# Optimization experiments

Hardware: AMD Instinct MI355X
Metric: run time of the kernel (lower is better)

## Reference

```python
import jax, jax.numpy as jnp
import numpy as np

T = 2048        # num tokens
HID = 2048      # hidden_size
HQ = 16         # num_heads
HKV = 8         # num_kv_heads
D = 128         # head_dim
P = 2           # power retention exponent
THETA = 10000.0 # rope base
SCALE = D ** -0.5


def setup_inputs() -> dict:
    key = jax.random.key(0)
    ks = jax.random.split(key, 8)
    s = 0.02
    return {
        "positions": jnp.arange(T, dtype=jnp.int64) if jax.config.jax_enable_x64 else jnp.arange(T, dtype=jnp.int32),
        "hidden_states": jax.random.normal(ks[0], (T, HID), jnp.float32),
        "Wq": jax.random.normal(ks[1], (HID, HQ * D), jnp.float32) * s,
        "bq": jnp.zeros((HQ * D,), jnp.float32),
        "Wk": jax.random.normal(ks[2], (HID, HKV * D), jnp.float32) * s,
        "bk": jnp.zeros((HKV * D,), jnp.float32),
        "Wv": jax.random.normal(ks[3], (HID, HKV * D), jnp.float32) * s,
        "bv": jnp.zeros((HKV * D,), jnp.float32),
        "Wg": jax.random.normal(ks[4], (HID, HKV), jnp.float32) * s,
        "bg": jnp.zeros((HKV,), jnp.float32),
        "Wo": jax.random.normal(ks[5], (HQ * D, HID), jnp.float32) * s,
        "bo": jnp.zeros((HID,), jnp.float32),
    }


def _rope_neox(x, pos):
    # x: [T, H, D], pos: [T]; rotate-half (neox) style, rotary_dim == head_dim
    half = D // 2
    inv_freq = 1.0 / (THETA ** (jnp.arange(0, D, 2, dtype=jnp.float32) / D))  # [D/2]
    freqs = pos.astype(jnp.float32)[:, None] * inv_freq                        # [T, D/2]
    cos = jnp.cos(freqs)[:, None, :]
    sin = jnp.sin(freqs)[:, None, :]
    x1, x2 = x[..., :half], x[..., half:]
    return jnp.concatenate([x1 * cos - x2 * sin, x2 * cos + x1 * sin], axis=-1)


def reference(positions, hidden_states, Wq, bq, Wk, bk, Wv, bv, Wg, bg, Wo, bo):
    # QKVG projections
    q = (hidden_states @ Wq + bq).reshape(T, HQ, D)
    k = (hidden_states @ Wk + bk).reshape(T, HKV, D)
    v = (hidden_states @ Wv + bv).reshape(T, HKV, D)
    g = hidden_states @ Wg + bg            # [T, HKV], one gate scalar per kv head

    # RoPE on q/k, logsigmoid gate in fp32
    q = _rope_neox(q, positions)
    k = _rope_neox(k, positions)
    g = jax.nn.log_sigmoid(g.astype(jnp.float32))   # [T, HKV], <= 0
    G = jnp.cumsum(g, axis=0)                       # [T, HKV] cumulative log-decay

    # GQA: expand kv heads to query heads
    rep = HQ // HKV
    k = jnp.repeat(k, rep, axis=1)   # [T, HQ, D]
    v = jnp.repeat(v, rep, axis=1)
    G = jnp.repeat(G, rep, axis=1)   # [T, HQ]

    # Power retention (quadratic attention form, seq_len <= switch_over_seq_len):
    # W_ij = (scale * q_i . k_j)^p * exp(G_i - G_j), causal j <= i
    S = jnp.einsum('thd,shd->hts', q, k) * SCALE      # [H, T, T]
    S = S ** P
    Gh = G.T                                          # [H, T]
    mask = jnp.tril(jnp.ones((T, T), dtype=bool))
    diff = jnp.where(mask[None], Gh[:, :, None] - Gh[:, None, :], -jnp.inf)
    W = S * jnp.exp(diff)                             # decay<=1 inside mask, 0 outside

    out = jnp.einsum('hts,shd->thd', W, v)            # [T, H, D]
    out = out.reshape(T, HQ * D) @ Wo + bo            # o_proj
    return out
```

## Files before the change

kernel.cpp:

```cpp
#include <hip/hip_runtime.h>
#include <hip/hip_bf16.h>
#include <math.h>

#define T_SEQ 2048
#define HID 2048
#define HQ 16
#define HKV 8
#define D_HEAD 128
#define HALF 64
#define SCALE_F 0.08838834764831845f
#define PROJW 4096

typedef __attribute__((ext_vector_type(8))) short bf16x8;
typedef __attribute__((ext_vector_type(4))) float f32x4;

static __device__ __forceinline__ short f2bf(float x) {
  unsigned u = __builtin_bit_cast(unsigned, x);
  unsigned r = (u + 0x7FFF + ((u >> 16) & 1)) >> 16;
  return (short)r;
}
static __device__ __forceinline__ float bf2f(unsigned short u) {
  unsigned v = ((unsigned)u) << 16;
  return __builtin_bit_cast(float, v);
}

#define GLDS(gsrc, ldst) \
  __builtin_amdgcn_global_load_lds((const __attribute__((address_space(1))) void*)(gsrc), \
                                   (__attribute__((address_space(3))) void*)(ldst), 16, 0, 0)

__global__ __launch_bounds__(256)
void transpose_all(const float* __restrict__ Wq, const float* __restrict__ Wk,
                   const float* __restrict__ Wv, const float* __restrict__ Wo,
                   short* __restrict__ BTall, short* __restrict__ WoT)
{
  const int bx = blockIdx.x;
  const int k0 = blockIdx.y * 32;
  const float* src; short* dst; int Nsrc, n0;
  if (bx < 64)       { src = Wq; Nsrc = 2048; dst = BTall;                       n0 = bx * 32; }
  else if (bx < 96)  { src = Wk; Nsrc = 1024; dst = BTall + (size_t)2048 * 2048; n0 = (bx - 64) * 32; }
  else if (bx < 128) { src = Wv; Nsrc = 1024; dst = BTall + (size_t)3072 * 2048; n0 = (bx - 96) * 32; }
  else               { src = Wo; Nsrc = 2048; dst = WoT;                         n0 = (bx - 128) * 32; }

  __shared__ float tile[32][33];
  const int r = threadIdx.x >> 5, c = threadIdx.x & 31;
  #pragma unroll
  for (int i = 0; i < 4; ++i)
    tile[r + i * 8][c] = src[(size_t)(k0 + r + i * 8) * Nsrc + n0 + c];
  __syncthreads();
  const int n = threadIdx.x >> 3, k4 = (threadIdx.x & 7) * 4;
  short4 o;
  o.x = f2bf(tile[k4 + 0][n]); o.y = f2bf(tile[k4 + 1][n]);
  o.z = f2bf(tile[k4 + 2][n]); o.w = f2bf(tile[k4 + 3][n]);
  *reinterpret_cast<short4*>(&dst[(size_t)(n0 + n) * 2048 + k0 + k4]) = o;
}

__global__ __launch_bounds__(256)
void add_f32(float* __restrict__ out, const float* __restrict__ part, int n4)
{
  int i = blockIdx.x * blockDim.x + threadIdx.x;
  if (i >= n4) return;
  float4 a = reinterpret_cast<float4*>(out)[i];
  const float4 b = reinterpret_cast<const float4*>(part)[i];
  a.x += b.x; a.y += b.y; a.z += b.z; a.w += b.w;
  reinterpret_cast<float4*>(out)[i] = a;
}

template <bool OBF>
__global__ __launch_bounds__(256)
void gemm_bf16(const short* __restrict__ A, const short* __restrict__ BT,
               const float* __restrict__ b0, const float* __restrict__ b1,
               const float* __restrict__ b2, int s1, int s2,
               void* __restrict__ Cout0, void* __restrict__ Cout1,
               int N, int Kst, int klen)
{
  __shared__ short As[2][128 * 32];
  __shared__ short Bs[2][128 * 32];
  const int tid = threadIdx.x;
  const int wave = tid >> 6, lane = tid & 63;
  const int bm0 = blockIdx.y * 128, bn0 = blockIdx.x * 128;
  const int z = blockIdx.z;
  const int koff = z * klen;
  const int wm = (wave >> 1) * 64, wn = (wave & 1) * 64;

  const int srow = wave * 32 + (lane >> 2);
  const int scol = (lane & 3) * 8;
  const short* Abase = A + (size_t)(bm0 + srow) * Kst + koff + scol;
  const short* Bbase = BT + (size_t)(bn0 + srow) * Kst + koff + scol;

  f32x4 acc[4][4] = {};

  const int nk = klen >> 5;
#define STAGE(buf, k0)                                                           \
  do {                                                                           \
    GLDS(Abase + (k0), &As[buf][(wave * 32) * 32]);                              \
    GLDS(Abase + (k0) + (size_t)16 * Kst, &As[buf][(wave * 32 + 16) * 32]);      \
    GLDS(Bbase + (k0), &Bs[buf][(wave * 32) * 32]);                              \
    GLDS(Bbase + (k0) + (size_t)16 * Kst, &Bs[buf][(wave * 32 + 16) * 32]);      \
  } while (0)

  STAGE(0, 0);
  __syncthreads();

  const int kof = (lane >> 4) * 8;
  const int rA = wm + (lane & 15);
  const int rB = wn + (lane & 15);

  for (int t = 0; t < nk; ++t) {
    const int cur = t & 1;
    if (t + 1 < nk) STAGE(cur ^ 1, (t + 1) << 5);
    bf16x8 af[4], bfr[4];
    #pragma unroll
    for (int i = 0; i < 4; ++i) {
      af[i]  = *reinterpret_cast<const bf16x8*>(&As[cur][(rA + i * 16) * 32 + kof]);
      bfr[i] = *reinterpret_cast<const bf16x8*>(&Bs[cur][(rB + i * 16) * 32 + kof]);
    }
    #pragma unroll
    for (int i = 0; i < 4; ++i)
      #pragma unroll
      for (int j = 0; j < 4; ++j)
        acc[i][j] = __builtin_amdgcn_mfma_f32_16x16x32_bf16(af[i], bfr[j], acc[i][j], 0, 0, 0);
    __syncthreads();
  }

  void* Cout = z ? Cout1 : Cout0;
  const int crow = wm + (lane >> 4) * 4;
  const int ccol = wn + (lane & 15);
  #pragma unroll
  for (int j = 0; j < 4; ++j) {
    const int col = bn0 + ccol + j * 16;
    float b = 0.f;
    if (z == 0)
      b = (col < s1) ? b0[col] : ((col < s2) ? b1[col - s1] : b2[col - s2]);
    #pragma unroll
    for (int i = 0; i < 4; ++i)
      #pragma unroll
      for (int r = 0; r < 4; ++r) {
        const int row = bm0 + crow + i * 16 + r;
        const float v = acc[i][j][r] + b;
        if (z == 0) {
          if constexpr (OBF)
            ((short*)Cout)[(size_t)row * N + col] = f2bf(v);
          else
            ((float*)Cout)[(size_t)row * N + col] = v;
        } else {
          ((float*)Cout)[(size_t)row * N + col] = v;
        }
      }
  }
#undef STAGE
}

__global__ __launch_bounds__(256)
void gproj_kernel(const float* __restrict__ hs, const float* __restrict__ Wg,
                  const float* __restrict__ bg, float* __restrict__ gT,
                  short* __restrict__ hsb)
{
  const int t = blockIdx.x, tid = threadIdx.x;
  __shared__ float red[256][9];
  float a[8] = {0.f, 0.f, 0.f, 0.f, 0.f, 0.f, 0.f, 0.f};
  for (int cc = tid; cc < HID; cc += 256) {
    const float hv = hs[(size_t)t * HID + cc];
    hsb[(size_t)t * HID + cc] = f2bf(hv);
    const float4 w0 = *reinterpret_cast<const float4*>(Wg + (size_t)cc * 8);
    const float4 w1 = *reinterpret_cast<const float4*>(Wg + (size_t)cc * 8 + 4);
    a[0] = fmaf(hv, w0.x, a[0]); a[1] = fmaf(hv, w0.y, a[1]);
    a[2] = fmaf(hv, w0.z, a[2]); a[3] = fmaf(hv, w0.w, a[3]);
    a[4] = fmaf(hv, w1.x, a[4]); a[5] = fmaf(hv, w1.y, a[5]);
    a[6] = fmaf(hv, w1.z, a[6]); a[7] = fmaf(hv, w1.w, a[7]);
  }
  #pragma unroll
  for (int j = 0; j < 8; ++j) red[tid][j] = a[j];
  __syncthreads();
  for (int s = 128; s >= 1; s >>= 1) {
    if (tid < s) {
      #pragma unroll
      for (int j = 0; j < 8; ++j) red[tid][j] += red[tid + s][j];
    }
    __syncthreads();
  }
  if (tid < 8) {
    const float x = red[0][tid] + bg[tid];
    const float nx = -x;
    const float sp = (nx > 20.f) ? nx : log1pf(expf(nx));
    gT[(size_t)tid * T_SEQ + t] = -sp;
  }
}

__global__ __launch_bounds__(512)
void gscan_kernel(const float* __restrict__ gT, float* __restrict__ Gct)
{
  const int h = blockIdx.x;
  const int tid = threadIdx.x;
  const int wid = tid >> 6, lane = tid & 63;
  __shared__ float wsum[8];

  const float4 v = reinterpret_cast<const float4*>(gT + (size_t)h * T_SEQ)[tid];
  const float p0 = v.x, p1 = p0 + v.y, p2 = p1 + v.z, p3 = p2 + v.w;

  float sc = p3;
  #pragma unroll
  for (int off = 1; off < 64; off <<= 1) {
    const float o = __shfl_up(sc, off, 64);
    if (lane >= off) sc += o;
  }
  if (lane == 63) wsum[wid] = sc;
  __syncthreads();
  float wof = 0.f;
  #pragma unroll
  for (int w = 0; w < 8; ++w) wof += (w < wid) ? wsum[w] : 0.f;

  const float excl = wof + sc - p3;
  reinterpret_cast<float4*>(Gct + (size_t)h * T_SEQ)[tid] =
      make_float4(excl + p0, excl + p1, excl + p2, excl + p3);
}

__global__ __launch_bounds__(256)
void rope_vtrans(short* __restrict__ proj, unsigned short* __restrict__ vt)
{
  __shared__ float cs[64], sn[64];
  __shared__ unsigned short tile[32][33];

  if (blockIdx.x < 2048) {
    const int t = blockIdx.x;
    if (threadIdx.x < 64) {
      const int i = threadIdx.x;
      const float f = (float)t * powf(10000.0f, -(float)i / 64.0f);
      cs[i] = cosf(f); sn[i] = sinf(f);
    }
    __syncthreads();
    const int u = threadIdx.x;
    if (u < 192) {
      const int hh = u >> 3, ch = u & 7;
      short* base = proj + (size_t)t * PROJW +
                    ((hh < HQ) ? hh * D_HEAD : 2048 + (hh - HQ) * D_HEAD);
      bf16x8 x1 = *reinterpret_cast<bf16x8*>(base + ch * 8);
      bf16x8 x2 = *reinterpret_cast<bf16x8*>(base + HALF + ch * 8);
      #pragma unroll
      for (int j = 0; j < 8; ++j) {
        const float a = bf2f((unsigned short)x1[j]);
        const float b = bf2f((unsigned short)x2[j]);
        const float cc = cs[ch * 8 + j], ss = sn[ch * 8 + j];
        x1[j] = f2bf(a * cc - b * ss);
        x2[j] = f2bf(b * cc + a * ss);
      }
      *reinterpret_cast<bf16x8*>(base + ch * 8) = x1;
      *reinterpret_cast<bf16x8*>(base + HALF + ch * 8) = x2;
    }
  } else {
    const int idx = blockIdx.x - 2048;
    const int tt = (idx & 63) * 32, dd = ((idx >> 6) & 3) * 32, hk = idx >> 8;
    const unsigned short* pj = (const unsigned short*)proj;
    const int c = threadIdx.x & 31, r0 = (threadIdx.x >> 5) * 4;
    #pragma unroll
    for (int i = 0; i < 4; ++i)
      tile[r0 + i][c] = pj[(size_t)(tt + r0 + i) * PROJW + 3072 + hk * 128 + dd + c];
    __syncthreads();
    #pragma unroll
    for (int i = 0; i < 4; ++i)
      vt[(size_t)(hk * 128 + dd + r0 + i) * T_SEQ + tt + c] = tile[c][r0 + i];
  }
}

__global__ __launch_bounds__(256, 1)
void attn_mfma(const short* __restrict__ proj, const short* __restrict__ vt,
               const float* __restrict__ Gct, short* __restrict__ outb)
{
  __shared__ __align__(16) char smem[86528];
  const int hk = blockIdx.x;
  const int tb = blockIdx.y * 64;
  const int tid = threadIdx.x;
  const int wid = tid >> 6, lane = tid & 63;
  const int c = lane & 15, g = lane >> 4;
  const int h = 2 * hk + (wid >> 1);
  const int tw = tb + (wid & 1) * 32;
  const float* Gh = Gct + (size_t)hk * T_SEQ;

  const float glim = Gh[tb] + 90.0f;
  int lo = 0, hi = tb;
  while (lo < hi) {
    const int mid = (lo + hi) >> 1;
    if (Gh[mid] > glim) lo = mid + 1; else hi = mid;
  }
  const int sfirst = lo & ~63;
  const int nst = ((tb - sfirst) >> 6) + 1;

  bf16x8 qf[2][4];
  #pragma unroll
  for (int tt = 0; tt < 2; ++tt)
    #pragma unroll
    for (int kb = 0; kb < 4; ++kb)
      qf[tt][kb] = *reinterpret_cast<const bf16x8*>(
          proj + (size_t)(tw + 16 * tt + c) * PROJW + h * D_HEAD + kb * 32 + g * 8);
  const float gt0 = Gh[tw + c];
  const float gt1 = Gh[tw + 16 + c];
  const float gtw = Gh[tw];
  const int twmax = tw + 31;

  f32x4 accv[2][8] = {};

#define ASTG(buf, s64)                                                                   \
  do {                                                                                   \
    _Pragma("unroll")                                                                    \
    for (int i2 = 0; i2 < 4; ++i2) {                                                     \
      const int cid = tid + 256 * i2;                                                    \
      const int kr = cid >> 4, kc = cid & 15;                                            \
      GLDS(proj + (size_t)((s64) + kr) * PROJW + 2048 + hk * 128 + ((kc ^ (kr & 7)) * 8),\
           smem + (buf) * 16384 + cid * 16);                                             \
      const int vr = cid >> 3, vc = cid & 7;                                             \
      GLDS(vt + (size_t)(hk * 128 + vr) * T_SEQ + (s64) + ((vc ^ (vr & 7)) * 8),         \
           smem + 32768 + (buf) * 16384 + cid * 16);                                     \
    }                                                                                    \
    if (tid < 64) ((float*)(smem + 86016))[(buf) * 64 + tid] = Gh[(s64) + tid];          \
  } while (0)

  ASTG(0, sfirst);
  __syncthreads();

  for (int i = 0; i < nst; ++i) {
    const int cur = i & 1;
    if (i + 1 < nst) ASTG(cur ^ 1, sfirst + (i + 1) * 64);
    const int sbase64 = sfirst + i * 64;
    const float* Gss = (const float*)(smem + 86016) + cur * 64;
    char* Pmy = smem + 65536 + wid * 5120;

    #pragma unroll
    for (int st = 0; st < 2; ++st) {
      const int s0 = sbase64 + st * 32;
      if (s0 > twmax) continue;
      if (gtw - Gss[st * 32 + 31] < -90.0f) continue;

      bf16x8 kf[2][4];
      #pragma unroll
      for (int sg = 0; sg < 2; ++sg)
        #pragma unroll
        for (int kb = 0; kb < 4; ++kb) {
          const int row = st * 32 + 16 * sg + c;
          const int byt = (row * 256 + kb * 64 + g * 16) ^ ((c & 7) << 4);
          kf[sg][kb] = *reinterpret_cast<const bf16x8*>(smem + cur * 16384 + byt);
        }
      f32x4 sa[2][2] = {};
      #pragma unroll
      for (int kb = 0; kb < 4; ++kb)
        #pragma unroll
        for (int sg = 0; sg < 2; ++sg)
          #pragma unroll
          for (int tt = 0; tt < 2; ++tt)
            sa[sg][tt] = __builtin_amdgcn_mfma_f32_16x16x32_bf16(
                kf[sg][kb], qf[tt][kb], sa[sg][tt], 0, 0, 0);

      #pragma unroll
      for (int sg = 0; sg < 2; ++sg) {
        const float4 gs = *reinterpret_cast<const float4*>(&Gss[st * 32 + sg * 16 + g * 4]);
        const float gsv[4] = {gs.x, gs.y, gs.z, gs.w};
        #pragma unroll
        for (int tt = 0; tt < 2; ++tt) {
          const int tg = tw + 16 * tt + c;
          const float gt = tt ? gt1 : gt0;
          const int sg0 = s0 + sg * 16 + g * 4;
          float w[4];
          #pragma unroll
          for (int r = 0; r < 4; ++r) {
            const float dv = sa[sg][tt][r] * SCALE_F;
            const float ww = dv * dv * __expf(gt - gsv[r]);
            w[r] = (sg0 + r <= tg) ? ww : 0.0f;
          }
          uint2 pv;
          pv.x = ((unsigned)(unsigned short)f2bf(w[1]) << 16) | (unsigned short)f2bf(w[0]);
          pv.y = ((unsigned)(unsigned short)f2bf(w[3]) << 16) | (unsigned short)f2bf(w[2]);
          *reinterpret_cast<uint2*>(Pmy + st * 2560 + (c + 16 * tt) * 80 + 8 * g + 32 * sg) = pv;
        }
      }
      asm volatile("s_waitcnt lgkmcnt(0)" ::: "memory");
      __builtin_amdgcn_sched_barrier(0);

      bf16x8 pf[2];
      #pragma unroll
      for (int tt = 0; tt < 2; ++tt)
        pf[tt] = *reinterpret_cast<const bf16x8*>(Pmy + st * 2560 + (c + 16 * tt) * 80 + g * 16);

      #pragma unroll
      for (int db = 0; db < 8; ++db) {
        const int row = 16 * db + c;
        const int byt = (row * 128 + st * 64 + g * 16) ^ ((c & 7) << 4);
        const bf16x8 vf = *reinterpret_cast<const bf16x8*>(smem + 32768 + cur * 16384 + byt);
        #pragma unroll
        for (int tt = 0; tt < 2; ++tt)
          accv[tt][db] = __builtin_amdgcn_mfma_f32_16x16x32_bf16(pf[tt], vf, accv[tt][db], 0, 0, 0);
      }
    }
    __syncthreads();
  }

  char* Wme = smem + wid * 8704;
  #pragma unroll
  for (int tt = 0; tt < 2; ++tt)
    #pragma unroll
    for (int db = 0; db < 8; ++db)
      #pragma unroll
      for (int r = 0; r < 4; ++r)
        *reinterpret_cast<short*>(Wme + (16 * tt + 4 * g + r) * 272 + (16 * db + c) * 2)
            = f2bf(accv[tt][db][r]);
  asm volatile("s_waitcnt lgkmcnt(0)" ::: "memory");
  __builtin_amdgcn_sched_barrier(0);
  #pragma unroll
  for (int e = 0; e < 8; ++e) {
    const int idx = e * 64 + lane;
    const int tr = idx >> 4, d0 = (idx & 15) * 8;
    const bf16x8 vv = *reinterpret_cast<const bf16x8*>(Wme + tr * 272 + d0 * 2);
    *reinterpret_cast<bf16x8*>(outb + ((size_t)(tw + tr) * HQ + h) * D_HEAD + d0) = vv;
  }
#undef ASTG
}

extern "C" void kernel_launch(void* const* d_in, const int* in_sizes, int n_in,
                              void* d_out, int out_size, void* d_ws, size_t ws_size,
                              hipStream_t stream)
{
  const float* hs = (const float*)d_in[1];
  const float* Wq = (const float*)d_in[2];
  const float* bq = (const float*)d_in[3];
  const float* Wk = (const float*)d_in[4];
  const float* bk = (const float*)d_in[5];
  const float* Wv = (const float*)d_in[6];
  const float* bv = (const float*)d_in[7];
  const float* Wg = (const float*)d_in[8];
  const float* bg = (const float*)d_in[9];
  const float* Wo = (const float*)d_in[10];
  const float* bo = (const float*)d_in[11];
  float* outp = (float*)d_out;

  short* proj  = (short*)d_ws;
  short* vtb   = proj + (size_t)T_SEQ * PROJW;
  float* gT    = (float*)(vtb + (size_t)HKV * D_HEAD * T_SEQ);
  float* Gct   = gT + 16384;
  short* hsb   = (short*)(Gct + 16384);
  short* BTall = hsb + (size_t)2048 * 2048;
  short* WoT   = BTall + (size_t)4096 * 2048;
  short* attnout = hsb;
  float* opart   = (float*)BTall;

  transpose_all<<<dim3(192, 64), 256, 0, stream>>>(Wq, Wk, Wv, Wo, BTall, WoT);

  gproj_kernel<<<2048, 256, 0, stream>>>(hs, Wg, bg, gT, hsb);
  gscan_kernel<<<8, 512, 0, stream>>>(gT, Gct);

  gemm_bf16<true><<<dim3(32, 16, 1), 256, 0, stream>>>(
      hsb, BTall, bq, bk, bv, 2048, 3072, proj, proj, PROJW, 2048, 2048);

  rope_vtrans<<<4096, 256, 0, stream>>>(proj, (unsigned short*)vtb);

  attn_mfma<<<dim3(8, 32), 256, 0, stream>>>(proj, vtb, Gct, attnout);

  gemm_bf16<false><<<dim3(16, 16, 2), 256, 0, stream>>>(
      attnout, WoT, bo, bo, bo, 1 << 30, 1 << 30, outp, opart, 2048, 2048, 1024);
  add_f32<<<4096, 256, 0, stream>>>(outp, opart, 1048576);
}
```

Before: 138.2 us.

## Split-K the QKV and O projections with bf16 partials folded in epilogue kernels

The QKV GEMM now runs as 2-way split-K. Its second partial is written in bf16 and added back inside a new fold+RoPE kernel, which also replaces the old combined rope/V-transpose kernel; the V transpose becomes its own kernel. The O projection becomes 4-way split-K with bf16 partials summed by an o_fold kernel, and the Wo transpose moves later so its buffer can reuse the space of the QKV weights. The aim is more blocks per GEMM to fill the CUs, at the cost of extra partial traffic, more launches and bf16 rounding of the partial sums.

```diff
diff --git a/kernel.cpp b/kernel.cpp
--- a/kernel.cpp
+++ b/kernel.cpp
@@ -29,17 +29,15 @@
                                    (__attribute__((address_space(3))) void*)(ldst), 16, 0, 0)
 
 __global__ __launch_bounds__(256)
-void transpose_all(const float* __restrict__ Wq, const float* __restrict__ Wk,
-                   const float* __restrict__ Wv, const float* __restrict__ Wo,
-                   short* __restrict__ BTall, short* __restrict__ WoT)
+void transpose_qkvw(const float* __restrict__ Wq, const float* __restrict__ Wk,
+                    const float* __restrict__ Wv, short* __restrict__ BTall)
 {
   const int bx = blockIdx.x;
   const int k0 = blockIdx.y * 32;
   const float* src; short* dst; int Nsrc, n0;
   if (bx < 64)       { src = Wq; Nsrc = 2048; dst = BTall;                       n0 = bx * 32; }
   else if (bx < 96)  { src = Wk; Nsrc = 1024; dst = BTall + (size_t)2048 * 2048; n0 = (bx - 64) * 32; }
-  else if (bx < 128) { src = Wv; Nsrc = 1024; dst = BTall + (size_t)3072 * 2048; n0 = (bx - 96) * 32; }
-  else               { src = Wo; Nsrc = 2048; dst = WoT;                         n0 = (bx - 128) * 32; }
+  else               { src = Wv; Nsrc = 1024; dst = BTall + (size_t)3072 * 2048; n0 = (bx - 96) * 32; }
 
   __shared__ float tile[32][33];
   const int r = threadIdx.x >> 5, c = threadIdx.x & 31;
@@ -55,14 +53,20 @@
 }
 
 __global__ __launch_bounds__(256)
-void add_f32(float* __restrict__ out, const float* __restrict__ part, int n4)
-{
-  int i = blockIdx.x * blockDim.x + threadIdx.x;
-  if (i >= n4) return;
-  float4 a = reinterpret_cast<float4*>(out)[i];
-  const float4 b = reinterpret_cast<const float4*>(part)[i];
-  a.x += b.x; a.y += b.y; a.z += b.z; a.w += b.w;
-  reinterpret_cast<float4*>(out)[i] = a;
+void transpose_wo(const float* __restrict__ Wo, short* __restrict__ WoT)
+{
+  const int k0 = blockIdx.y * 32, n0 = blockIdx.x * 32;
+  __shared__ float tile[32][33];
+  const int r = threadIdx.x >> 5, c = threadIdx.x & 31;
+  #pragma unroll
+  for (int i = 0; i < 4; ++i)
+    tile[r + i * 8][c] = Wo[(size_t)(k0 + r + i * 8) * 2048 + n0 + c];
+  __syncthreads();
+  const int n = threadIdx.x >> 3, k4 = (threadIdx.x & 7) * 4;
+  short4 o;
+  o.x = f2bf(tile[k4 + 0][n]); o.y = f2bf(tile[k4 + 1][n]);
+  o.z = f2bf(tile[k4 + 2][n]); o.w = f2bf(tile[k4 + 3][n]);
+  *reinterpret_cast<short4*>(&WoT[(size_t)(n0 + n) * 2048 + k0 + k4]) = o;
 }
 
 template <bool OBF>
@@ -70,7 +74,8 @@
 void gemm_bf16(const short* __restrict__ A, const short* __restrict__ BT,
                const float* __restrict__ b0, const float* __restrict__ b1,
                const float* __restrict__ b2, int s1, int s2,
-               void* __restrict__ Cout0, void* __restrict__ Cout1,
+               void* __restrict__ Cout0, short* __restrict__ P1,
+               short* __restrict__ P2, short* __restrict__ P3,
                int N, int Kst, int klen)
 {
   __shared__ short As[2][128 * 32];
@@ -122,9 +127,9 @@
     __syncthreads();
   }
 
-  void* Cout = z ? Cout1 : Cout0;
   const int crow = wm + (lane >> 4) * 4;
   const int ccol = wn + (lane & 15);
+  short* P = (z == 1) ? P1 : ((z == 2) ? P2 : P3);
   #pragma unroll
   for (int j = 0; j < 4; ++j) {
     const int col = bn0 + ccol + j * 16;
@@ -139,11 +144,11 @@
         const float v = acc[i][j][r] + b;
         if (z == 0) {
           if constexpr (OBF)
-            ((short*)Cout)[(size_t)row * N + col] = f2bf(v);
+            ((short*)Cout0)[(size_t)row * N + col] = f2bf(v);
           else
-            ((float*)Cout)[(size_t)row * N + col] = v;
+            ((float*)Cout0)[(size_t)row * N + col] = v;
         } else {
-          ((float*)Cout)[(size_t)row * N + col] = v;
+          P[(size_t)row * N + col] = f2bf(v);
         }
       }
   }
@@ -215,50 +220,75 @@
 }
 
 __global__ __launch_bounds__(256)
-void rope_vtrans(short* __restrict__ proj, unsigned short* __restrict__ vt)
-{
+void qkv_fold_rope(short* __restrict__ proj, const short* __restrict__ part1)
+{
+  const int t = blockIdx.x;
   __shared__ float cs[64], sn[64];
+  if (threadIdx.x < 64) {
+    const int i = threadIdx.x;
+    const float f = (float)t * powf(10000.0f, -(float)i / 64.0f);
+    cs[i] = cosf(f); sn[i] = sinf(f);
+  }
+  __syncthreads();
+
+  const int ch = ((threadIdx.x >> 3) << 4) + (threadIdx.x & 7);
+  const size_t base = (size_t)t * PROJW + ch * 8;
+  bf16x8 a1 = *reinterpret_cast<bf16x8*>(proj + base);
+  bf16x8 a2 = *reinterpret_cast<bf16x8*>(proj + base + 64);
+  const bf16x8 q1 = *reinterpret_cast<const bf16x8*>(part1 + base);
+  const bf16x8 q2 = *reinterpret_cast<const bf16x8*>(part1 + base + 64);
+  const int head = ch >> 4;
+  const int i0 = (ch & 7) * 8;
+  #pragma unroll
+  for (int j = 0; j < 8; ++j) {
+    const float x1 = bf2f((unsigned short)a1[j]) + bf2f((unsigned short)q1[j]);
+    const float x2 = bf2f((unsigned short)a2[j]) + bf2f((unsigned short)q2[j]);
+    if (head < 24) {
+      const float cc = cs[i0 + j], ss = sn[i0 + j];
+      a1[j] = f2bf(x1 * cc - x2 * ss);
+      a2[j] = f2bf(x2 * cc + x1 * ss);
+    } else {
+      a1[j] = f2bf(x1);
+      a2[j] = f2bf(x2);
+    }
+  }
+  *reinterpret_cast<bf16x8*>(proj + base) = a1;
+  *reinterpret_cast<bf16x8*>(proj + base + 64) = a2;
+}
+
+__global__ __launch_bounds__(256)
+void vtrans_kernel(const unsigned short* __restrict__ proj, unsigned short* __restrict__ vt)
+{
   __shared__ unsigned short tile[32][33];
-
-  if (blockIdx.x < 2048) {
-    const int t = blockIdx.x;
-    if (threadIdx.x < 64) {
-      const int i = threadIdx.x;
-      const float f = (float)t * powf(10000.0f, -(float)i / 64.0f);
-      cs[i] = cosf(f); sn[i] = sinf(f);
-    }
-    __syncthreads();
-    const int u = threadIdx.x;
-    if (u < 192) {
-      const int hh = u >> 3, ch = u & 7;
-      short* base = proj + (size_t)t * PROJW +
-                    ((hh < HQ) ? hh * D_HEAD : 2048 + (hh - HQ) * D_HEAD);
-      bf16x8 x1 = *reinterpret_cast<bf16x8*>(base + ch * 8);
-      bf16x8 x2 = *reinterpret_cast<bf16x8*>(base + HALF + ch * 8);
-      #pragma unroll
-      for (int j = 0; j < 8; ++j) {
-        const float a = bf2f((unsigned short)x1[j]);
-        const float b = bf2f((unsigned short)x2[j]);
-        const float cc = cs[ch * 8 + j], ss = sn[ch * 8 + j];
-        x1[j] = f2bf(a * cc - b * ss);
-        x2[j] = f2bf(b * cc + a * ss);
-      }
-      *reinterpret_cast<bf16x8*>(base + ch * 8) = x1;
-      *reinterpret_cast<bf16x8*>(base + HALF + ch * 8) = x2;
-    }
-  } else {
-    const int idx = blockIdx.x - 2048;
-    const int tt = (idx & 63) * 32, dd = ((idx >> 6) & 3) * 32, hk = idx >> 8;
-    const unsigned short* pj = (const unsigned short*)proj;
-    const int c = threadIdx.x & 31, r0 = (threadIdx.x >> 5) * 4;
-    #pragma unroll
-    for (int i = 0; i < 4; ++i)
-      tile[r0 + i][c] = pj[(size_t)(tt + r0 + i) * PROJW + 3072 + hk * 128 + dd + c];
-    __syncthreads();
-    #pragma unroll
-    for (int i = 0; i < 4; ++i)
-      vt[(size_t)(hk * 128 + dd + r0 + i) * T_SEQ + tt + c] = tile[c][r0 + i];
-  }
+  const int tt = blockIdx.x * 32, dd = blockIdx.y * 32, hk = blockIdx.z;
+  const int c = threadIdx.x & 31, r0 = (threadIdx.x >> 5) * 4;
+  #pragma unroll
+  for (int i = 0; i < 4; ++i)
+    tile[r0 + i][c] = proj[(size_t)(tt + r0 + i) * PROJW + 3072 + hk * 128 + dd + c];
+  __syncthreads();
+  #pragma unroll
+  for (int i = 0; i < 4; ++i)
+    vt[(size_t)(hk * 128 + dd + r0 + i) * T_SEQ + tt + c] = tile[c][r0 + i];
+}
+
+__global__ __launch_bounds__(256)
+void o_fold(float* __restrict__ out, const short* __restrict__ p1,
+            const short* __restrict__ p2, const short* __restrict__ p3)
+{
+  const size_t i = ((size_t)blockIdx.x * 256 + threadIdx.x) * 8;
+  const bf16x8 a = *reinterpret_cast<const bf16x8*>(p1 + i);
+  const bf16x8 b = *reinterpret_cast<const bf16x8*>(p2 + i);
+  const bf16x8 cc = *reinterpret_cast<const bf16x8*>(p3 + i);
+  float4 o0 = *reinterpret_cast<float4*>(out + i);
+  float4 o1 = *reinterpret_cast<float4*>(out + i + 4);
+  float s[8];
+  #pragma unroll
+  for (int j = 0; j < 8; ++j)
+    s[j] = bf2f((unsigned short)a[j]) + bf2f((unsigned short)b[j]) + bf2f((unsigned short)cc[j]);
+  o0.x += s[0]; o0.y += s[1]; o0.z += s[2]; o0.w += s[3];
+  o1.x += s[4]; o1.y += s[5]; o1.z += s[6]; o1.w += s[7];
+  *reinterpret_cast<float4*>(out + i) = o0;
+  *reinterpret_cast<float4*>(out + i + 4) = o1;
 }
 
 __global__ __launch_bounds__(256, 1)
@@ -435,23 +465,34 @@
   float* Gct   = gT + 16384;
   short* hsb   = (short*)(Gct + 16384);
   short* BTall = hsb + (size_t)2048 * 2048;
-  short* WoT   = BTall + (size_t)4096 * 2048;
+  short* part1 = BTall + (size_t)4096 * 2048;
+  short* WoT     = BTall;
   short* attnout = hsb;
-  float* opart   = (float*)BTall;
-
-  transpose_all<<<dim3(192, 64), 256, 0, stream>>>(Wq, Wk, Wv, Wo, BTall, WoT);
+  short* opart1  = part1;
+  short* opart2  = part1 + (size_t)2048 * 2048;
+  short* opart3  = proj;
+
+  transpose_qkvw<<<dim3(128, 64), 256, 0, stream>>>(Wq, Wk, Wv, BTall);
 
   gproj_kernel<<<2048, 256, 0, stream>>>(hs, Wg, bg, gT, hsb);
   gscan_kernel<<<8, 512, 0, stream>>>(gT, Gct);
 
-  gemm_bf16<true><<<dim3(32, 16, 1), 256, 0, stream>>>(
-      hsb, BTall, bq, bk, bv, 2048, 3072, proj, proj, PROJW, 2048, 2048);
-
-  rope_vtrans<<<4096, 256, 0, stream>>>(proj, (unsigned short*)vtb);
+  gemm_bf16<true><<<dim3(32, 16, 2), 256, 0, stream>>>(
+      hsb, BTall, bq, bk, bv, 2048, 3072, proj, part1, part1, part1,
+      PROJW, 2048, 1024);
+
+  qkv_fold_rope<<<2048, 256, 0, stream>>>(proj, part1);
+
+  vtrans_kernel<<<dim3(64, 4, 8), 256, 0, stream>>>((const unsigned short*)proj,
+                                                    (unsigned short*)vtb);
+
+  transpose_wo<<<dim3(64, 64), 256, 0, stream>>>(Wo, WoT);
 
   attn_mfma<<<dim3(8, 32), 256, 0, stream>>>(proj, vtb, Gct, attnout);
 
-  gemm_bf16<false><<<dim3(16, 16, 2), 256, 0, stream>>>(
-      attnout, WoT, bo, bo, bo, 1 << 30, 1 << 30, outp, opart, 2048, 2048, 1024);
-  add_f32<<<4096, 256, 0, stream>>>(outp, opart, 1048576);
-}
+  gemm_bf16<false><<<dim3(16, 16, 4), 256, 0, stream>>>(
+      attnout, WoT, bo, bo, bo, 1 << 30, 1 << 30, outp, opart1, opart2, opart3,
+      2048, 2048, 512);
+
+  o_fold<<<2048, 256, 0, stream>>>(outp, opart1, opart2, opart3);
+}
```

Measured after the change: 159.4 us. +15.4%, slower.
